# Kernel tuning notes

Hardware: AMD Instinct MI355X
Metric: run time of the kernel (lower is better)

Reference implementation:

```python
import jax, jax.numpy as jnp
import numpy as np

B, S, D, H, DK, DV = 4, 1024, 1024, 16, 64, 64
EPS = 1e-6


def _cv_layernorm(xr, xi, g_rr, g_ri, g_ii, b_r, b_i):
    # complex layernorm via 2x2 covariance whitening (Deep Complex Networks style)
    mr = xr.mean(-1, keepdims=True)
    mi = xi.mean(-1, keepdims=True)
    r = xr - mr
    i = xi - mi
    Vrr = (r * r).mean(-1, keepdims=True) + EPS
    Vii = (i * i).mean(-1, keepdims=True) + EPS
    Vri = (r * i).mean(-1, keepdims=True)
    s = jnp.sqrt(Vrr * Vii - Vri * Vri)        # sqrt(det V)
    t = jnp.sqrt(Vrr + Vii + 2.0 * s)
    inv = 1.0 / (s * t)
    Wrr = (Vii + s) * inv
    Wii = (Vrr + s) * inv
    Wri = -Vri * inv
    or_ = Wrr * r + Wri * i
    oi = Wri * r + Wii * i
    return g_rr * or_ + g_ri * oi + b_r, g_ri * or_ + g_ii * oi + b_i


def _forward(q_r, q_i, k_r, k_i, v_r, v_i, wq_r, wq_i, wk_r, wk_i, wv_r, wv_i,
             fc_r, fc_i, gamma_rr, gamma_ri, gamma_ii, beta_r, beta_i):
    qc_in = (q_r + 1j * q_i).astype(jnp.complex64)
    kc = (k_r + 1j * k_i).astype(jnp.complex64)
    vc = (v_r + 1j * v_i).astype(jnp.complex64)
    wq = (wq_r + 1j * wq_i).astype(jnp.complex64)
    wk = (wk_r + 1j * wk_i).astype(jnp.complex64)
    wv = (wv_r + 1j * wv_i).astype(jnp.complex64)
    fc = (fc_r + 1j * fc_i).astype(jnp.complex64)

    # complex QKV projections (torch Linear: y = x @ W.T), split into heads
    q = (qc_in @ wq.T).reshape(B, S, H, DK).transpose(0, 2, 1, 3)  # [B,H,S,DK]
    k = (kc @ wk.T).reshape(B, S, H, DK).transpose(0, 2, 1, 3)
    v = (vc @ wv.T).reshape(B, S, H, DV).transpose(0, 2, 1, 3)

    temp = jnp.float32(DK ** 0.5)
    attn = jnp.einsum('bhqd,bhkd->bhqk', q / temp, k)  # complex [B,H,S,S]

    # MagMinMaxNorm over last dim: min-max normalize magnitude, keep phase
    mag = jnp.abs(attn)
    mn = mag.min(-1, keepdims=True)
    mx = mag.max(-1, keepdims=True)
    scale = (mag - mn) / ((mx - mn) * mag + 1e-12)
    attn = attn * scale

    o = jnp.einsum('bhqk,bhkd->bhqd', attn, v)
    o = o.transpose(0, 2, 1, 3).reshape(B, S, H * DV)  # [B,S,H*DV]
    o = o @ fc.T
    o = o + qc_in  # residual
    out_r, out_i = _cv_layernorm(o.real, o.imag, gamma_rr, gamma_ri, gamma_ii, beta_r, beta_i)
    return jnp.stack([out_r, out_i])  # [2,B,S,D]


def setup_inputs() -> dict:
    key = jax.random.key(0)
    ks = jax.random.split(key, 14)
    rn = lambda k, shape, sc=1.0: jax.random.normal(k, shape, jnp.float32) * sc
    ws = 1.0 / np.sqrt(D)
    return {
        'q_r': rn(ks[0], (B, S, D)), 'q_i': rn(ks[1], (B, S, D)),
        'k_r': rn(ks[2], (B, S, D)), 'k_i': rn(ks[3], (B, S, D)),
        'v_r': rn(ks[4], (B, S, D)), 'v_i': rn(ks[5], (B, S, D)),
        'wq_r': rn(ks[6], (H * DK, D), ws), 'wq_i': rn(ks[7], (H * DK, D), ws),
        'wk_r': rn(ks[8], (H * DK, D), ws), 'wk_i': rn(ks[9], (H * DK, D), ws),
        'wv_r': rn(ks[10], (H * DV, D), ws), 'wv_i': rn(ks[11], (H * DV, D), ws),
        'fc_r': rn(ks[12], (D, H * DV), ws), 'fc_i': rn(ks[13], (D, H * DV), ws),
        'gamma_rr': jnp.ones((D,), jnp.float32), 'gamma_ri': jnp.zeros((D,), jnp.float32),
        'gamma_ii': jnp.ones((D,), jnp.float32),
        'beta_r': jnp.zeros((D,), jnp.float32), 'beta_i': jnp.zeros((D,), jnp.float32),
    }


def reference(q_r, q_i, k_r, k_i, v_r, v_i, wq_r, wq_i, wk_r, wk_i, wv_r, wv_i,
              fc_r, fc_i, gamma_rr, gamma_ri, gamma_ii, beta_r, beta_i):
    return _forward(q_r, q_i, k_r, k_i, v_r, v_i, wq_r, wq_i, wk_r, wk_i, wv_r, wv_i,
                    fc_r, fc_i, gamma_rr, gamma_ri, gamma_ii, beta_r, beta_i)
```

## Files before the change

### kernel.cpp

```cpp
#include <hip/hip_runtime.h>
#include <hip/hip_bf16.h>

#define BB 4
#define SS 1024
#define DD 1024
#define HH 16
#define DKH 64
#define EPS_LN 1e-6f

#define M_ROWS 4096
#define KK 2048

typedef float  floatx4 __attribute__((ext_vector_type(4)));
typedef short  shortx8 __attribute__((ext_vector_type(8)));
#define MFMA16(a, b, c) __builtin_amdgcn_mfma_f32_16x16x32_bf16(a, b, c, 0, 0, 0)

__device__ __forceinline__ unsigned pk2(float lo, float hi) {
    unsigned u;
    asm("v_cvt_pk_bf16_f32 %0, %1, %2" : "=v"(u) : "v"(lo), "v"(hi));
    return u;
}

__device__ __forceinline__ ushort f2b(float x) {
    return (ushort)(pk2(x, x) & 0xffffu);
}

__device__ __forceinline__ shortx8 negf(shortx8 x) {
    shortx8 r;
    #pragma unroll
    for (int i = 0; i < 8; ++i) r[i] = (short)(x[i] ^ (short)0x8000);
    return r;
}

__device__ __forceinline__ shortx8 vswap(shortx8 v) {
    union { shortx8 s; unsigned u[4]; } a, b;
    a.s = v;
    #pragma unroll
    for (int i = 0; i < 4; ++i) {
        const unsigned w = a.u[i];
        b.u[i] = ((w >> 16) | (w << 16)) ^ 0x00008000u;
    }
    return b.s;
}

__device__ __forceinline__ void gl16(const void* g, void* l) {
    __builtin_amdgcn_global_load_lds(
        (const __attribute__((address_space(1))) unsigned int*)g,
        (__attribute__((address_space(3))) unsigned int*)l, 16, 0, 0);
}

__global__ __launch_bounds__(256) void pack_x(
    const float* __restrict__ qr, const float* __restrict__ qi,
    const float* __restrict__ kr, const float* __restrict__ ki,
    const float* __restrict__ vr, const float* __restrict__ vi,
    ushort* __restrict__ Xq, ushort* __restrict__ Xk, ushort* __restrict__ Xv)
{
    const int t = blockIdx.y;
    const float* pr = t == 0 ? qr : t == 1 ? kr : vr;
    const float* pi = t == 0 ? qi : t == 1 ? ki : vi;
    ushort* X = t == 0 ? Xq : t == 1 ? Xk : Xv;
    const int idx = blockIdx.x * 256 + threadIdx.x;
    const int row = idx >> 8, c4 = (idx & 255) * 4;
    float4 a = *(const float4*)(pr + (size_t)row * 1024 + c4);
    float4 b = *(const float4*)(pi + (size_t)row * 1024 + c4);
    ushort4 ua; ua.x = f2b(a.x); ua.y = f2b(a.y); ua.z = f2b(a.z); ua.w = f2b(a.w);
    ushort4 ub; ub.x = f2b(b.x); ub.y = f2b(b.y); ub.z = f2b(b.z); ub.w = f2b(b.w);
    *(ushort4*)(X + (size_t)row * KK + c4)        = ua;
    *(ushort4*)(X + (size_t)row * KK + 1024 + c4) = ub;
}

__global__ __launch_bounds__(256) void pack_w(
    const float* __restrict__ ar, const float* __restrict__ ai,
    const float* __restrict__ br, const float* __restrict__ bi,
    const float* __restrict__ cr, const float* __restrict__ ci,
    const float* __restrict__ dr, const float* __restrict__ di,
    ushort* __restrict__ Bq, ushort* __restrict__ Bk,
    ushort* __restrict__ Bv, ushort* __restrict__ Bf)
{
    const int t = blockIdx.y;
    const float* wr = t == 0 ? ar : t == 1 ? br : t == 2 ? cr : dr;
    const float* wi = t == 0 ? ai : t == 1 ? bi : t == 2 ? ci : di;
    ushort* Bo = t == 0 ? Bq : t == 1 ? Bk : t == 2 ? Bv : Bf;
    const int idx = blockIdx.x * 256 + threadIdx.x;
    const int n = idx >> 8, c4 = (idx & 255) * 4;
    float4 a = *(const float4*)(wr + (size_t)n * 1024 + c4);
    float4 b = *(const float4*)(wi + (size_t)n * 1024 + c4);
    ushort4 ua; ua.x = f2b(a.x);  ua.y = f2b(a.y);  ua.z = f2b(a.z);  ua.w = f2b(a.w);
    ushort4 ub; ub.x = f2b(b.x);  ub.y = f2b(b.y);  ub.z = f2b(b.z);  ub.w = f2b(b.w);
    ushort4 un; un.x = f2b(-b.x); un.y = f2b(-b.y); un.z = f2b(-b.z); un.w = f2b(-b.w);
    *(ushort4*)(Bo + (size_t)n * KK + c4)                 = ua;
    *(ushort4*)(Bo + (size_t)n * KK + 1024 + c4)          = un;
    *(ushort4*)(Bo + (size_t)(1024 + n) * KK + c4)        = ub;
    *(ushort4*)(Bo + (size_t)(1024 + n) * KK + 1024 + c4) = ua;
}

#define GBM 128
#define GBN 256
#define GBK 64

#define GSTAGE(P, KT) do {                                                    \
    const ushort* ga_ = gA + (KT) * GBK;                                      \
    const ushort* gb_ = gB + (KT) * GBK;                                      \
    ushort* la_ = &As[P][st8];                                                \
    ushort* lb_ = &Bs[P][st8];                                                \
    gl16(ga_,                la_);                                            \
    gl16(ga_ + 64 * KK,      la_ + 4096);                                     \
    gl16(gb_,                lb_);                                            \
    gl16(gb_ + 64 * KK,      lb_ + 4096);                                     \
    gl16(gb_ + 128 * KK,     lb_ + 8192);                                     \
    gl16(gb_ + 192 * KK,     lb_ + 12288);                                    \
} while (0)

#define GKSTEP(P, VM, DOSTAGE) do {                                           \
    asm volatile("s_waitcnt vmcnt(" #VM ")" ::: "memory");                    \
    __builtin_amdgcn_s_barrier();                                             \
    __builtin_amdgcn_sched_barrier(0);                                        \
    const ushort* Ap = As[P];                                                 \
    const ushort* Bp = Bs[P];                                                 \
    shortx8 a[4][2], b[4][2];                                                 \
    _Pragma("unroll")                                                         \
    for (int f = 0; f < 4; ++f) {                                             \
        const int ra = (wm + f * 16 + l15) * GBK;                             \
        const int rb = (wn + f * 16 + l15) * GBK;                             \
        a[f][0] = *(const shortx8*)&Ap[ra + ca0];                             \
        a[f][1] = *(const shortx8*)&Ap[ra + ca1];                             \
        b[f][0] = *(const shortx8*)&Bp[rb + ca0];                             \
        b[f][1] = *(const shortx8*)&Bp[rb + ca1];                             \
    }                                                                         \
    __builtin_amdgcn_s_setprio(1);                                            \
    _Pragma("unroll")                                                         \
    for (int fm = 0; fm < 4; ++fm)                                            \
        _Pragma("unroll")                                                     \
        for (int fn = 0; fn < 4; ++fn) {                                      \
            acc[fm][fn] = MFMA16(a[fm][0], b[fn][0], acc[fm][fn]);            \
            acc[fm][fn] = MFMA16(a[fm][1], b[fn][1], acc[fm][fn]);            \
        }                                                                     \
    __builtin_amdgcn_s_setprio(0);                                            \
    asm volatile("s_waitcnt lgkmcnt(0)" ::: "memory");                        \
    __builtin_amdgcn_sched_barrier(0);                                        \
    __builtin_amdgcn_s_barrier();                                             \
    if (DOSTAGE) GSTAGE(P, kt + 2);                                           \
    ++kt;                                                                     \
} while (0)

__device__ __forceinline__ void bgemm_body(
    const ushort* __restrict__ A, const ushort* __restrict__ Bm,
    void* __restrict__ out0, void* __restrict__ out1,
    const float* __restrict__ resr, const float* __restrict__ resi,
    float scale, int mode, int bx, int by)
{
    __shared__ __align__(16) ushort As[2][GBM * GBK];
    __shared__ __align__(16) ushort Bs[2][GBN * GBK];

    const int t = threadIdx.x;
    const int lane = t & 63, wave = t >> 6;
    const int l15 = lane & 15, quad = lane >> 4;
    const int wm = (wave >> 2) * 64;
    const int wn = (wave & 3) * 64;
    const int m0 = by * GBM, n0 = bx * GBN;

    const int srow = t >> 3;
    const int schk = (t & 7) ^ (srow & 7);
    const int st8  = t * 8;
    const ushort* gA = A  + (size_t)(m0 + srow) * KK + schk * 8;
    const ushort* gB = Bm + (size_t)(n0 + srow) * KK + schk * 8;

    const int rm  = l15 & 7;
    const int ca0 = ((quad)     ^ rm) * 8;
    const int ca1 = ((4 + quad) ^ rm) * 8;

    floatx4 acc[4][4];
    #pragma unroll
    for (int fm = 0; fm < 4; ++fm)
        #pragma unroll
        for (int fn = 0; fn < 4; ++fn)
            acc[fm][fn] = (floatx4){0.f, 0.f, 0.f, 0.f};

    GSTAGE(0, 0);
    GSTAGE(1, 1);

    int kt = 0;
    for (int i = 0; i < 15; ++i) {
        GKSTEP(0, 6, 1);
        GKSTEP(1, 6, 1);
    }
    GKSTEP(0, 6, 0);
    GKSTEP(1, 0, 0);

    #pragma unroll
    for (int fm = 0; fm < 4; ++fm) {
        #pragma unroll
        for (int fn = 0; fn < 4; ++fn) {
            #pragma unroll
            for (int r = 0; r < 4; ++r) {
                const int m = m0 + wm + fm * 16 + quad * 4 + r;
                const int n = n0 + wn + fn * 16 + l15;
                const float v = acc[fm][fn][r] * scale;
                const int nn = n & 1023;
                const int hh = nn >> 6;
                const int bb = m >> 10, s = m & 1023;
                if (mode == 0) {
                    const int dk = (n < 1024 ? 0 : 64) + (nn & 63);
                    const int tq = s >> 5, row = s & 31;
                    ushort* Qb = (ushort*)out0 +
                        ((size_t)(bb * HH + hh) * 32 + tq) * 4096;
                    const int off = ((row >> 4) * 4 + (dk >> 5)) * 512 +
                                    ((dk >> 3) & 3) * 128 + (row & 15) * 8 + (dk & 7);
                    Qb[off] = f2b(v);
                } else if (mode == 3) {
                    const int dk = (n < 1024 ? 0 : 64) + (nn & 63);
                    const int tt = s >> 6, row = s & 63;
                    ushort* Kb = (ushort*)out0 +
                        ((size_t)(bb * HH + hh) * 16 + tt) * 8192;
                    const int off = ((row >> 4) * 4 + (dk >> 5)) * 512 +
                                    ((dk >> 3) & 3) * 128 + (row & 15) * 8 + (dk & 7);
                    Kb[off] = f2b(v);
                } else if (mode == 1) {
                    const int dv = nn & 63;
                    const int c = 2 * s + (n < 1024 ? 0 : 1);
                    ushort* Vb = (ushort*)out0 + (size_t)(bb * HH + hh) * 131072;
                    const int off = (((c >> 7) * 4 + (dv >> 4)) * 4 + ((c >> 5) & 3)) * 512 +
                                    ((c >> 3) & 3) * 128 + (dv & 15) * 8 + (c & 7);
                    Vb[off] = f2b(n < 1024 ? v : -v);
                } else {
                    const size_t off = (size_t)m * 1024 + nn;
                    if (n < 1024) ((float*)out0)[off] = v + resr[off];
                    else          ((float*)out1)[off] = v + resi[off];
                }
            }
        }
    }
}

__global__ __launch_bounds__(512) void bgemm_qk(
    const ushort* __restrict__ Xq, const ushort* __restrict__ Xk,
    const ushort* __restrict__ Bq, const ushort* __restrict__ Bk,
    ushort* __restrict__ qpk, ushort* __restrict__ kpk)
{
    const int z = blockIdx.z;
    bgemm_body(z == 0 ? Xq : Xk, z == 0 ? Bq : Bk,
               z == 0 ? (void*)qpk : (void*)kpk, nullptr, nullptr, nullptr,
               z == 0 ? 0.125f : 1.0f, z == 0 ? 0 : 3, blockIdx.x, blockIdx.y);
}

__global__ __launch_bounds__(512) void bgemm_v(
    const ushort* __restrict__ Xv, const ushort* __restrict__ Bv,
    ushort* __restrict__ Vneg)
{
    bgemm_body(Xv, Bv, (void*)Vneg, nullptr, nullptr, nullptr,
               1.0f, 1, blockIdx.x, blockIdx.y);
}

__global__ __launch_bounds__(512) void bgemm_fc(
    const ushort* __restrict__ A, const ushort* __restrict__ Bm,
    float* __restrict__ fr, float* __restrict__ fi,
    const float* __restrict__ resr, const float* __restrict__ resi)
{
    bgemm_body(A, Bm, fr, fi, resr, resi, 1.0f, 2, blockIdx.x, blockIdx.y);
}

#define SWZ(row, col) (((row) << 5) + ((col) ^ (((row) & 7) << 2)))

__device__ __forceinline__ void loadK(shortx8 (&K)[2][4], const ushort* kfb,
                                      int t, int kt_w) {
    #pragma unroll
    for (int kt2 = 0; kt2 < 2; ++kt2)
        #pragma unroll
        for (int f = 0; f < 4; ++f)
            K[kt2][f] = *(const shortx8*)(kfb + t * 8192 +
                                          ((kt_w * 2 + kt2) * 4 + f) * 512);
}

__device__ __forceinline__ void loadVn(shortx8 (&V)[4], const ushort* vfb,
                                       int t, int wave) {
    #pragma unroll
    for (int f = 0; f < 4; ++f)
        V[f] = *(const shortx8*)(vfb + ((t * 4 + wave) * 4 + f) * 512);
}

#define ATTN_ITER(IT, NX, KC, KN)                                             \
  {                                                                           \
    loadVn(V_, vfb, (IT), wave);                                              \
    const int p_ = (IT) & 1;                                                  \
    unsigned* Ab = Abuf[p_][kt_w];                                            \
    unsigned* Pb = Pbuf[p_][kt_w];                                            \
    floatx4 cr[2], ci[2];                                                     \
    _Pragma("unroll")                                                         \
    for (int kt2 = 0; kt2 < 2; ++kt2) {                                       \
      floatx4 r_ = (floatx4){0.f, 0.f, 0.f, 0.f};                             \
      floatx4 i_ = (floatx4){0.f, 0.f, 0.f, 0.f};                             \
      r_ = MFMA16(Aq0, KC[kt2][0], r_); r_ = MFMA16(Aq1, KC[kt2][1], r_);     \
      r_ = MFMA16(Nq2, KC[kt2][2], r_); r_ = MFMA16(Nq3, KC[kt2][3], r_);     \
      i_ = MFMA16(Aq2, KC[kt2][0], i_); i_ = MFMA16(Aq3, KC[kt2][1], i_);     \
      i_ = MFMA16(Aq0, KC[kt2][2], i_); i_ = MFMA16(Aq1, KC[kt2][3], i_);     \
      cr[kt2] = r_; ci[kt2] = i_;                                             \
    }                                                                         \
    loadK(KN, kfb, (NX), kt_w);                                               \
    _Pragma("unroll")                                                         \
    for (int kt2 = 0; kt2 < 2; ++kt2) {                                       \
      _Pragma("unroll")                                                       \
      for (int r = 0; r < 4; ++r) {                                           \
        const float ar = cr[kt2][r], ai = ci[kt2][r];                         \
        const float s2 = fmaf(ar, ar, ai * ai);                               \
        const float irm = s2 > 0.f ? rsqrtf(s2) : 0.f;                        \
        const float mag = s2 * irm;                                           \
        rmn[r] = fminf(rmn[r], mag);                                          \
        rmx[r] = fmaxf(rmx[r], mag);                                          \
        const int row_ = qt_w * 16 + quad * 4 + r;                            \
        const int w_ = SWZ(row_, kt2 * 16 + l15);                             \
        Ab[w_] = pk2(ar, ai);                                                 \
        Pb[w_] = pk2(ar * irm, ai * irm);                                     \
      }                                                                       \
    }                                                                         \
    asm volatile("s_waitcnt lgkmcnt(0)" ::: "memory");                        \
    __builtin_amdgcn_s_barrier();                                             \
    const shortx8 Vs0 = vswap(V_[0]), Vs1 = vswap(V_[1]);                     \
    const shortx8 Vs2 = vswap(V_[2]), Vs3 = vswap(V_[3]);                     \
    const unsigned* A0 = Abuf[p_][0];                                         \
    const unsigned* A1 = Abuf[p_][1];                                         \
    const unsigned* P0 = Pbuf[p_][0];                                         \
    const unsigned* P1 = Pbuf[p_][1];                                         \
    __builtin_amdgcn_s_setprio(1);                                            \
    _Pragma("unroll")                                                         \
    for (int q2 = 0; q2 < 2; ++q2) {                                          \
      const int row_ = q2 * 16 + l15;                                         \
      const int rb_ = row_ * 32, rm_ = (row_ & 7) << 2;                       \
      const int c0_ = rb_ + ((quad * 4) ^ rm_);                               \
      const int c1_ = rb_ + ((16 + quad * 4) ^ rm_);                          \
      shortx8 Af0 = *(const shortx8*)&A0[c0_];                                \
      shortx8 Af1 = *(const shortx8*)&A0[c1_];                                \
      shortx8 Af2 = *(const shortx8*)&A1[c0_];                                \
      shortx8 Af3 = *(const shortx8*)&A1[c1_];                                \
      shortx8 Pf0 = *(const shortx8*)&P0[c0_];                                \
      shortx8 Pf1 = *(const shortx8*)&P0[c1_];                                \
      shortx8 Pf2 = *(const shortx8*)&P1[c0_];                                \
      shortx8 Pf3 = *(const shortx8*)&P1[c1_];                                \
      acc[q2][0] = MFMA16(Af0, V_[0], acc[q2][0]);                            \
      acc[q2][0] = MFMA16(Af1, V_[1], acc[q2][0]);                            \
      acc[q2][0] = MFMA16(Af2, V_[2], acc[q2][0]);                            \
      acc[q2][0] = MFMA16(Af3, V_[3], acc[q2][0]);                            \
      acc[q2][1] = MFMA16(Af0, Vs0, acc[q2][1]);                              \
      acc[q2][1] = MFMA16(Af1, Vs1, acc[q2][1]);                              \
      acc[q2][1] = MFMA16(Af2, Vs2, acc[q2][1]);                              \
      acc[q2][1] = MFMA16(Af3, Vs3, acc[q2][1]);                              \
      acc[q2][2] = MFMA16(Pf0, V_[0], acc[q2][2]);                            \
      acc[q2][2] = MFMA16(Pf1, V_[1], acc[q2][2]);                            \
      acc[q2][2] = MFMA16(Pf2, V_[2], acc[q2][2]);                            \
      acc[q2][2] = MFMA16(Pf3, V_[3], acc[q2][2]);                            \
      acc[q2][3] = MFMA16(Pf0, Vs0, acc[q2][3]);                              \
      acc[q2][3] = MFMA16(Pf1, Vs1, acc[q2][3]);                              \
      acc[q2][3] = MFMA16(Pf2, Vs2, acc[q2][3]);                              \
      acc[q2][3] = MFMA16(Pf3, Vs3, acc[q2][3]);                              \
    }                                                                         \
    __builtin_amdgcn_s_setprio(0);                                            \
  }

__global__ __launch_bounds__(256) void attn_mfma(
    const ushort* __restrict__ qpk, const ushort* __restrict__ kpk,
    const ushort* __restrict__ vn, ushort* __restrict__ xo)
{
    __shared__ unsigned Abuf[2][2][32 * 32];
    __shared__ unsigned Pbuf[2][2][32 * 32];
    __shared__ unsigned mnb[32], mxb[32];

    const int tid  = threadIdx.x;
    const int wave = tid >> 6, lane = tid & 63;
    const int l15  = lane & 15, quad = lane >> 4;
    const int qt_w = wave & 1, kt_w = wave >> 1;

    const int swz = (blockIdx.x & 7) * 256 + (blockIdx.x >> 3);
    const int qt = swz & 31, hb = swz >> 5;
    const int h = hb & 15, b = hb >> 4;
    const size_t qrow0 = (size_t)b * SS + (size_t)qt * 32;

    if (tid < 32) { mnb[tid] = 0x7f800000u; mxb[tid] = 0u; }

    const ushort* qfb = qpk + ((size_t)(b * HH + h) * 32 + qt) * 4096 + lane * 8;
    shortx8 Aq0 = *(const shortx8*)(qfb + (qt_w * 4 + 0) * 512);
    shortx8 Aq1 = *(const shortx8*)(qfb + (qt_w * 4 + 1) * 512);
    shortx8 Aq2 = *(const shortx8*)(qfb + (qt_w * 4 + 2) * 512);
    shortx8 Aq3 = *(const shortx8*)(qfb + (qt_w * 4 + 3) * 512);
    shortx8 Nq2 = negf(Aq2), Nq3 = negf(Aq3);

    const ushort* kfb = kpk + (size_t)(b * HH + h) * 131072 + lane * 8;
    const ushort* vfb = vn  + (size_t)(b * HH + h) * 131072 + lane * 8;

    floatx4 acc[2][4];
    #pragma unroll
    for (int q2 = 0; q2 < 2; ++q2)
        #pragma unroll
        for (int j = 0; j < 4; ++j)
            acc[q2][j] = (floatx4){0.f, 0.f, 0.f, 0.f};
    float rmn[4] = {1e30f, 1e30f, 1e30f, 1e30f};
    float rmx[4] = {0.f, 0.f, 0.f, 0.f};

    shortx8 KA[2][4], KB[2][4], V_[4];
    loadK(KA, kfb, 0, kt_w);

    for (int it = 0; it < 16; it += 2) {
        ATTN_ITER(it,     it + 1,        KA, KB);
        ATTN_ITER(it + 1, (it + 2) & 15, KB, KA);
    }

    #pragma unroll
    for (int r = 0; r < 4; ++r) {
        float mn = rmn[r], mx = rmx[r];
        #pragma unroll
        for (int o = 1; o < 16; o <<= 1) {
            mn = fminf(mn, __shfl_xor(mn, o));
            mx = fmaxf(mx, __shfl_xor(mx, o));
        }
        if (l15 == 0) {
            const int q = qt_w * 16 + quad * 4 + r;
            atomicMin(&mnb[q], __float_as_uint(mn));
            atomicMax(&mxb[q], __float_as_uint(mx));
        }
    }
    __syncthreads();

    #pragma unroll
    for (int q2 = 0; q2 < 2; ++q2) {
        #pragma unroll
        for (int r = 0; r < 4; ++r) {
            const int q = q2 * 16 + quad * 4 + r;
            const float mn = __uint_as_float(mnb[q]);
            const float mx = __uint_as_float(mxb[q]);
            const float d = mx - mn;
            const float invd = d > 0.f ? 1.f / d : 0.f;
            const float vr_ = (acc[q2][0][r] - mn * acc[q2][2][r]) * invd;
            const float vi_ = (acc[q2][1][r] - mn * acc[q2][3][r]) * invd;
            const size_t row = (qrow0 + q) * KK + h * 64 + wave * 16 + l15;
            xo[row]        = f2b(vr_);
            xo[row + 1024] = f2b(vi_);
        }
    }
}

__global__ __launch_bounds__(256) void ln_kernel(
    const float* __restrict__ xr, const float* __restrict__ xi,
    const float* __restrict__ g_rr, const float* __restrict__ g_ri,
    const float* __restrict__ g_ii,
    const float* __restrict__ b_r, const float* __restrict__ b_i,
    float* __restrict__ out)
{
    const int lane = threadIdx.x & 63;
    const int wave = threadIdx.x >> 6;
    const int row  = blockIdx.x * 4 + wave;
    const float* pr = xr + (size_t)row * DD;
    const float* pi = xi + (size_t)row * DD;

    float r[16], im[16];
    float sr = 0.f, si = 0.f;
    #pragma unroll
    for (int j = 0; j < 16; ++j) {
        r[j]  = pr[lane + 64*j];
        im[j] = pi[lane + 64*j];
        sr += r[j]; si += im[j];
    }
    #pragma unroll
    for (int o = 32; o; o >>= 1) { sr += __shfl_xor(sr, o); si += __shfl_xor(si, o); }
    const float mr = sr * (1.f / DD), mi = si * (1.f / DD);

    float srr = 0.f, sii = 0.f, sri = 0.f;
    #pragma unroll
    for (int j = 0; j < 16; ++j) {
        const float a = r[j] - mr, c = im[j] - mi;
        srr = fmaf(a, a, srr); sii = fmaf(c, c, sii); sri = fmaf(a, c, sri);
    }
    #pragma unroll
    for (int o = 32; o; o >>= 1) {
        srr += __shfl_xor(srr, o); sii += __shfl_xor(sii, o); sri += __shfl_xor(sri, o);
    }
    const float Vrr = srr * (1.f / DD) + EPS_LN;
    const float Vii = sii * (1.f / DD) + EPS_LN;
    const float Vri = sri * (1.f / DD);
    const float s  = sqrtf(Vrr * Vii - Vri * Vri);
    const float t  = sqrtf(Vrr + Vii + 2.f * s);
    const float inv = 1.f / (s * t);
    const float Wrr = (Vii + s) * inv;
    const float Wii = (Vrr + s) * inv;
    const float Wri = -Vri * inv;

    #pragma unroll
    for (int j = 0; j < 16; ++j) {
        const int d = lane + 64*j;
        const float a = r[j] - mr, c = im[j] - mi;
        const float or_ = Wrr * a + Wri * c;
        const float oi_ = Wri * a + Wii * c;
        out[(size_t)row * DD + d] = g_rr[d]*or_ + g_ri[d]*oi_ + b_r[d];
        out[(size_t)(M_ROWS) * DD + (size_t)row * DD + d] = g_ri[d]*or_ + g_ii[d]*oi_ + b_i[d];
    }
}

extern "C" void kernel_launch(void* const* d_in, const int* in_sizes, int n_in,
                              void* d_out, int out_size, void* d_ws, size_t ws_size,
                              hipStream_t stream) {
    const float* q_r  = (const float*)d_in[0];
    const float* q_i  = (const float*)d_in[1];
    const float* k_r  = (const float*)d_in[2];
    const float* k_i  = (const float*)d_in[3];
    const float* v_r  = (const float*)d_in[4];
    const float* v_i  = (const float*)d_in[5];
    const float* wq_r = (const float*)d_in[6];
    const float* wq_i = (const float*)d_in[7];
    const float* wk_r = (const float*)d_in[8];
    const float* wk_i = (const float*)d_in[9];
    const float* wv_r = (const float*)d_in[10];
    const float* wv_i = (const float*)d_in[11];
    const float* fc_r = (const float*)d_in[12];
    const float* fc_i = (const float*)d_in[13];
    const float* g_rr = (const float*)d_in[14];
    const float* g_ri = (const float*)d_in[15];
    const float* g_ii = (const float*)d_in[16];
    const float* b_r  = (const float*)d_in[17];
    const float* b_i  = (const float*)d_in[18];
    float* out = (float*)d_out;

    float* ws = (float*)d_ws;
    const size_t NE = (size_t)M_ROWS * 1024;
    ushort* Xq   = (ushort*)(ws + 0 * NE);
    ushort* Xk   = (ushort*)(ws + 1 * NE);
    ushort* Xv   = (ushort*)(ws + 2 * NE);
    ushort* qpk  = (ushort*)(ws + 3 * NE);
    ushort* kpk  = (ushort*)(ws + 4 * NE);
    ushort* Bq   = (ushort*)(ws + 5 * NE);
    ushort* Bk   = Bq + (size_t)KK * KK;
    ushort* Bv   = (ushort*)(ws + 6 * NE);
    ushort* Bf   = Bv + (size_t)KK * KK;
    ushort* Vneg = (ushort*)(ws + 0 * NE);
    ushort* xo   = (ushort*)(ws + 2 * NE);
    float*  fr   = ws + 3 * NE;
    float*  fi   = ws + 4 * NE;

    pack_x<<<dim3(4096, 3), 256, 0, stream>>>(q_r, q_i, k_r, k_i, v_r, v_i, Xq, Xk, Xv);
    pack_w<<<dim3(1024, 4), 256, 0, stream>>>(wq_r, wq_i, wk_r, wk_i, wv_r, wv_i,
                                              fc_r, fc_i, Bq, Bk, Bv, Bf);

    bgemm_qk<<<dim3(KK / GBN, M_ROWS / GBM, 2), 512, 0, stream>>>(
        Xq, Xk, Bq, Bk, qpk, kpk);

    bgemm_v<<<dim3(KK / GBN, M_ROWS / GBM), 512, 0, stream>>>(Xv, Bv, Vneg);

    attn_mfma<<<dim3(2048), 256, 0, stream>>>(qpk, kpk, Vneg, xo);

    bgemm_fc<<<dim3(KK / GBN, M_ROWS / GBM), 512, 0, stream>>>(xo, Bf, fr, fi, q_r, q_i);

    ln_kernel<<<M_ROWS / 4, 256, 0, stream>>>(fr, fi, g_rr, g_ri, g_ii, b_r, b_i, out);
}
```

Baseline: 509.0 us.

## Enlarge GEMM tile to 256x256 with phased LDS reads and fuse QKV launch

```diff
diff --git a/kernel.cpp b/kernel.cpp
--- a/kernel.cpp
+++ b/kernel.cpp
@@ -94,52 +94,100 @@
     *(ushort4*)(Bo + (size_t)(1024 + n) * KK + 1024 + c4) = ua;
 }
 
-#define GBM 128
+#define GBM 256
 #define GBN 256
 #define GBK 64
 
-#define GSTAGE(P, KT) do {                                                    \
-    const ushort* ga_ = gA + (KT) * GBK;                                      \
-    const ushort* gb_ = gB + (KT) * GBK;                                      \
+#define STAGE8(P, T) do {                                                     \
+    const ushort* ga_ = gA + (size_t)(T) * GBK;                               \
+    const ushort* gb_ = gB + (size_t)(T) * GBK;                               \
     ushort* la_ = &As[P][st8];                                                \
     ushort* lb_ = &Bs[P][st8];                                                \
-    gl16(ga_,                la_);                                            \
-    gl16(ga_ + 64 * KK,      la_ + 4096);                                     \
-    gl16(gb_,                lb_);                                            \
-    gl16(gb_ + 64 * KK,      lb_ + 4096);                                     \
-    gl16(gb_ + 128 * KK,     lb_ + 8192);                                     \
-    gl16(gb_ + 192 * KK,     lb_ + 12288);                                    \
+    _Pragma("unroll")                                                         \
+    for (int s_ = 0; s_ < 4; ++s_)                                            \
+        gl16(ga_ + (size_t)s_ * 64 * KK, la_ + s_ * 4096);                    \
+    _Pragma("unroll")                                                         \
+    for (int s_ = 0; s_ < 4; ++s_)                                            \
+        gl16(gb_ + (size_t)s_ * 64 * KK, lb_ + s_ * 4096);                    \
 } while (0)
 
-#define GKSTEP(P, VM, DOSTAGE) do {                                           \
+#define TILE8(P, VM, DOSTAGE) do {                                            \
     asm volatile("s_waitcnt vmcnt(" #VM ")" ::: "memory");                    \
     __builtin_amdgcn_s_barrier();                                             \
+                                                                 \
+    _Pragma("unroll")                                                         \
+    for (int j = 0; j < 4; ++j) {                                             \
+        const int ra_ = aoff + j * 1024;                                      \
+        aA[j][0] = *(const shortx8*)&As[P][ra_ + ca0];                        \
+        aA[j][1] = *(const shortx8*)&As[P][ra_ + ca1];                        \
+    }                                                                         \
+    _Pragma("unroll")                                                         \
+    for (int j = 0; j < 2; ++j) {                                             \
+        const int rb_ = boff + j * 1024;                                      \
+        bA[j][0] = *(const shortx8*)&Bs[P][rb_ + ca0];                        \
+        bA[j][1] = *(const shortx8*)&Bs[P][rb_ + ca1];                        \
+    }                                                                         \
+    asm volatile("s_waitcnt lgkmcnt(0)" ::: "memory");                        \
     __builtin_amdgcn_sched_barrier(0);                                        \
-    const ushort* Ap = As[P];                                                 \
-    const ushort* Bp = Bs[P];                                                 \
-    shortx8 a[4][2], b[4][2];                                                 \
-    _Pragma("unroll")                                                         \
-    for (int f = 0; f < 4; ++f) {                                             \
-        const int ra = (wm + f * 16 + l15) * GBK;                             \
-        const int rb = (wn + f * 16 + l15) * GBK;                             \
-        a[f][0] = *(const shortx8*)&Ap[ra + ca0];                             \
-        a[f][1] = *(const shortx8*)&Ap[ra + ca1];                             \
-        b[f][0] = *(const shortx8*)&Bp[rb + ca0];                             \
-        b[f][1] = *(const shortx8*)&Bp[rb + ca1];                             \
-    }                                                                         \
     __builtin_amdgcn_s_setprio(1);                                            \
     _Pragma("unroll")                                                         \
-    for (int fm = 0; fm < 4; ++fm)                                            \
+    for (int j = 0; j < 4; ++j)                                               \
         _Pragma("unroll")                                                     \
-        for (int fn = 0; fn < 4; ++fn) {                                      \
-            acc[fm][fn] = MFMA16(a[fm][0], b[fn][0], acc[fm][fn]);            \
-            acc[fm][fn] = MFMA16(a[fm][1], b[fn][1], acc[fm][fn]);            \
+        for (int n_ = 0; n_ < 2; ++n_) {                                      \
+            acc[j][n_] = MFMA16(aA[j][0], bA[n_][0], acc[j][n_]);             \
+            acc[j][n_] = MFMA16(aA[j][1], bA[n_][1], acc[j][n_]);             \
         }                                                                     \
     __builtin_amdgcn_s_setprio(0);                                            \
+    __builtin_amdgcn_s_barrier();                                             \
+                                                                 \
+    _Pragma("unroll")                                                         \
+    for (int j = 0; j < 2; ++j) {                                             \
+        const int rb_ = boff + 2048 + j * 1024;                               \
+        bB[j][0] = *(const shortx8*)&Bs[P][rb_ + ca0];                        \
+        bB[j][1] = *(const shortx8*)&Bs[P][rb_ + ca1];                        \
+    }                                                                         \
     asm volatile("s_waitcnt lgkmcnt(0)" ::: "memory");                        \
     __builtin_amdgcn_sched_barrier(0);                                        \
+    __builtin_amdgcn_s_setprio(1);                                            \
+    _Pragma("unroll")                                                         \
+    for (int j = 0; j < 4; ++j)                                               \
+        _Pragma("unroll")                                                     \
+        for (int n_ = 0; n_ < 2; ++n_) {                                      \
+            acc[j][2 + n_] = MFMA16(aA[j][0], bB[n_][0], acc[j][2 + n_]);     \
+            acc[j][2 + n_] = MFMA16(aA[j][1], bB[n_][1], acc[j][2 + n_]);     \
+        }                                                                     \
+    __builtin_amdgcn_s_setprio(0);                                            \
     __builtin_amdgcn_s_barrier();                                             \
-    if (DOSTAGE) GSTAGE(P, kt + 2);                                           \
+                                                                 \
+    _Pragma("unroll")                                                         \
+    for (int j = 0; j < 4; ++j) {                                             \
+        const int ra_ = aoff + 4096 + j * 1024;                               \
+        aA[j][0] = *(const shortx8*)&As[P][ra_ + ca0];                        \
+        aA[j][1] = *(const shortx8*)&As[P][ra_ + ca1];                        \
+    }                                                                         \
+    asm volatile("s_waitcnt lgkmcnt(0)" ::: "memory");                        \
+    __builtin_amdgcn_sched_barrier(0);                                        \
+    __builtin_amdgcn_s_setprio(1);                                            \
+    _Pragma("unroll")                                                         \
+    for (int j = 0; j < 4; ++j)                                               \
+        _Pragma("unroll")                                                     \
+        for (int n_ = 0; n_ < 2; ++n_) {                                      \
+            acc[4 + j][2 + n_] = MFMA16(aA[j][0], bB[n_][0], acc[4 + j][2 + n_]); \
+            acc[4 + j][2 + n_] = MFMA16(aA[j][1], bB[n_][1], acc[4 + j][2 + n_]); \
+        }                                                                     \
+    __builtin_amdgcn_s_setprio(0);                                            \
+    __builtin_amdgcn_s_barrier();                                             \
+                     \
+    if (DOSTAGE) STAGE8(P, kt + 2);                                           \
+    __builtin_amdgcn_s_setprio(1);                                            \
+    _Pragma("unroll")                                                         \
+    for (int j = 0; j < 4; ++j)                                               \
+        _Pragma("unroll")                                                     \
+        for (int n_ = 0; n_ < 2; ++n_) {                                      \
+            acc[4 + j][n_] = MFMA16(aA[j][0], bA[n_][0], acc[4 + j][n_]);     \
+            acc[4 + j][n_] = MFMA16(aA[j][1], bA[n_][1], acc[4 + j][n_]);     \
+        }                                                                     \
+    __builtin_amdgcn_s_setprio(0);                                            \
     ++kt;                                                                     \
 } while (0)
 
@@ -155,7 +203,7 @@
     const int t = threadIdx.x;
     const int lane = t & 63, wave = t >> 6;
     const int l15 = lane & 15, quad = lane >> 4;
-    const int wm = (wave >> 2) * 64;
+    const int wm = (wave >> 2) * 128;
     const int wn = (wave & 3) * 64;
     const int m0 = by * GBM, n0 = bx * GBN;
 
@@ -168,27 +216,31 @@
     const int rm  = l15 & 7;
     const int ca0 = ((quad)     ^ rm) * 8;
     const int ca1 = ((4 + quad) ^ rm) * 8;
-
-    floatx4 acc[4][4];
-    #pragma unroll
-    for (int fm = 0; fm < 4; ++fm)
+    const int aoff = (wm + l15) * 64;
+    const int boff = (wn + l15) * 64;
+
+    floatx4 acc[8][4];
+    #pragma unroll
+    for (int fm = 0; fm < 8; ++fm)
         #pragma unroll
         for (int fn = 0; fn < 4; ++fn)
             acc[fm][fn] = (floatx4){0.f, 0.f, 0.f, 0.f};
 
-    GSTAGE(0, 0);
-    GSTAGE(1, 1);
+    shortx8 aA[4][2], bA[2][2], bB[2][2];
+
+    STAGE8(0, 0);
+    STAGE8(1, 1);
 
     int kt = 0;
     for (int i = 0; i < 15; ++i) {
-        GKSTEP(0, 6, 1);
-        GKSTEP(1, 6, 1);
-    }
-    GKSTEP(0, 6, 0);
-    GKSTEP(1, 0, 0);
-
-    #pragma unroll
-    for (int fm = 0; fm < 4; ++fm) {
+        TILE8(0, 8, 1);
+        TILE8(1, 8, 1);
+    }
+    TILE8(0, 8, 0);
+    TILE8(1, 0, 0);
+
+    #pragma unroll
+    for (int fm = 0; fm < 8; ++fm) {
         #pragma unroll
         for (int fn = 0; fn < 4; ++fn) {
             #pragma unroll
@@ -232,23 +284,22 @@
     }
 }
 
-__global__ __launch_bounds__(512) void bgemm_qk(
+__global__ __launch_bounds__(512) void bgemm_qkv(
     const ushort* __restrict__ Xq, const ushort* __restrict__ Xk,
+    const ushort* __restrict__ Xv,
     const ushort* __restrict__ Bq, const ushort* __restrict__ Bk,
-    ushort* __restrict__ qpk, ushort* __restrict__ kpk)
+    const ushort* __restrict__ Bv,
+    ushort* __restrict__ qpk, ushort* __restrict__ kpk,
+    ushort* __restrict__ Vneg)
 {
     const int z = blockIdx.z;
-    bgemm_body(z == 0 ? Xq : Xk, z == 0 ? Bq : Bk,
-               z == 0 ? (void*)qpk : (void*)kpk, nullptr, nullptr, nullptr,
-               z == 0 ? 0.125f : 1.0f, z == 0 ? 0 : 3, blockIdx.x, blockIdx.y);
-}
-
-__global__ __launch_bounds__(512) void bgemm_v(
-    const ushort* __restrict__ Xv, const ushort* __restrict__ Bv,
-    ushort* __restrict__ Vneg)
-{
-    bgemm_body(Xv, Bv, (void*)Vneg, nullptr, nullptr, nullptr,
-               1.0f, 1, blockIdx.x, blockIdx.y);
+    const ushort* A  = z == 0 ? Xq : z == 1 ? Xk : Xv;
+    const ushort* Bm = z == 0 ? Bq : z == 1 ? Bk : Bv;
+    void* o0 = z == 0 ? (void*)qpk : z == 1 ? (void*)kpk : (void*)Vneg;
+    const float sc = z == 0 ? 0.125f : 1.0f;
+    const int mode = z == 0 ? 0 : z == 1 ? 3 : 1;
+    bgemm_body(A, Bm, o0, nullptr, nullptr, nullptr, sc, mode,
+               blockIdx.x, blockIdx.y);
 }
 
 __global__ __launch_bounds__(512) void bgemm_fc(
@@ -527,7 +578,7 @@
     ushort* Bk   = Bq + (size_t)KK * KK;
     ushort* Bv   = (ushort*)(ws + 6 * NE);
     ushort* Bf   = Bv + (size_t)KK * KK;
-    ushort* Vneg = (ushort*)(ws + 0 * NE);
+    ushort* Vneg = (ushort*)d_out;
     ushort* xo   = (ushort*)(ws + 2 * NE);
     float*  fr   = ws + 3 * NE;
     float*  fi   = ws + 4 * NE;
@@ -536,10 +587,8 @@
     pack_w<<<dim3(1024, 4), 256, 0, stream>>>(wq_r, wq_i, wk_r, wk_i, wv_r, wv_i,
                                               fc_r, fc_i, Bq, Bk, Bv, Bf);
 
-    bgemm_qk<<<dim3(KK / GBN, M_ROWS / GBM, 2), 512, 0, stream>>>(
-        Xq, Xk, Bq, Bk, qpk, kpk);
-
-    bgemm_v<<<dim3(KK / GBN, M_ROWS / GBM), 512, 0, stream>>>(Xv, Bv, Vneg);
+    bgemm_qkv<<<dim3(KK / GBN, M_ROWS / GBM, 3), 512, 0, stream>>>(
+        Xq, Xk, Xv, Bq, Bk, Bv, qpk, kpk, Vneg);
 
     attn_mfma<<<dim3(2048), 256, 0, stream>>>(qpk, kpk, Vneg, xo);
 
```

After: 530.1 us. +4.1%, slower.

## Deepen GEMM pipeline to 4 stages with register double-buffering and merge QKV launches

Applied to the files above, without the earlier changes.

```diff
diff --git a/kernel.cpp b/kernel.cpp
--- a/kernel.cpp
+++ b/kernel.cpp
@@ -94,53 +94,51 @@
     *(ushort4*)(Bo + (size_t)(1024 + n) * KK + 1024 + c4) = ua;
 }
 
-#define GBM 128
-#define GBN 256
-#define GBK 64
-
-#define GSTAGE(P, KT) do {                                                    \
-    const ushort* ga_ = gA + (KT) * GBK;                                      \
-    const ushort* gb_ = gB + (KT) * GBK;                                      \
-    ushort* la_ = &As[P][st8];                                                \
-    ushort* lb_ = &Bs[P][st8];                                                \
-    gl16(ga_,                la_);                                            \
-    gl16(ga_ + 64 * KK,      la_ + 4096);                                     \
-    gl16(gb_,                lb_);                                            \
-    gl16(gb_ + 64 * KK,      lb_ + 4096);                                     \
-    gl16(gb_ + 128 * KK,     lb_ + 8192);                                     \
-    gl16(gb_ + 192 * KK,     lb_ + 12288);                                    \
+#define GBM 256
+#define GBN 128
+#define GBK 32
+#define ASLOT (GBM * GBK)
+#define BSLOT (GBN * GBK)
+
+#define GSTG(S) do {                                                          \
+    const int sl_ = (S) & 3;                                                  \
+    const ushort* ga_ = gA0 + (S) * GBK;                                      \
+    const ushort* gb_ = gB0 + (S) * GBK;                                      \
+    ushort* la_ = AsAll + sl_ * ASLOT + t8;                                   \
+    ushort* lb_ = BsAll + sl_ * BSLOT + t8;                                   \
+    gl16(ga_, la_);                                                           \
+    gl16(ga_ + 128 * KK, la_ + 4096);                                         \
+    gl16(gb_, lb_);                                                           \
 } while (0)
 
-#define GKSTEP(P, VM, DOSTAGE) do {                                           \
+#define GRD(J, AN, BN) do {                                                   \
+    const ushort* As_ = AsAll + ((J) & 3) * ASLOT + ard;                      \
+    const ushort* Bs_ = BsAll + ((J) & 3) * BSLOT + brd;                      \
+    AN[0] = *(const shortx8*)(As_);                                           \
+    AN[1] = *(const shortx8*)(As_ + 16 * GBK);                                \
+    AN[2] = *(const shortx8*)(As_ + 32 * GBK);                                \
+    AN[3] = *(const shortx8*)(As_ + 48 * GBK);                                \
+    BN[0] = *(const shortx8*)(Bs_);                                           \
+    BN[1] = *(const shortx8*)(Bs_ + 16 * GBK);                                \
+    BN[2] = *(const shortx8*)(Bs_ + 32 * GBK);                                \
+    BN[3] = *(const shortx8*)(Bs_ + 48 * GBK);                                \
+} while (0)
+
+#define GBODY(J, VM, DOSTAGE, DOREAD, AC, BC, AN, BN) do {                    \
+    if (DOREAD) GRD((J) + 1, AN, BN);                                         \
+    if (DOSTAGE) GSTG((J) + 4);                                               \
+    __builtin_amdgcn_sched_barrier(0);                                        \
+    __builtin_amdgcn_s_setprio(1);                                            \
+    _Pragma("unroll")                                                         \
+    for (int f_ = 0; f_ < 4; ++f_)                                            \
+        _Pragma("unroll")                                                     \
+        for (int g_ = 0; g_ < 4; ++g_)                                        \
+            acc[f_][g_] = MFMA16(AC[f_], BC[g_], acc[f_][g_]);                \
+    __builtin_amdgcn_s_setprio(0);                                            \
+    __builtin_amdgcn_sched_barrier(0);                                        \
+    asm volatile("s_waitcnt lgkmcnt(0)" ::: "memory");                        \
     asm volatile("s_waitcnt vmcnt(" #VM ")" ::: "memory");                    \
     __builtin_amdgcn_s_barrier();                                             \
-    __builtin_amdgcn_sched_barrier(0);                                        \
-    const ushort* Ap = As[P];                                                 \
-    const ushort* Bp = Bs[P];                                                 \
-    shortx8 a[4][2], b[4][2];                                                 \
-    _Pragma("unroll")                                                         \
-    for (int f = 0; f < 4; ++f) {                                             \
-        const int ra = (wm + f * 16 + l15) * GBK;                             \
-        const int rb = (wn + f * 16 + l15) * GBK;                             \
-        a[f][0] = *(const shortx8*)&Ap[ra + ca0];                             \
-        a[f][1] = *(const shortx8*)&Ap[ra + ca1];                             \
-        b[f][0] = *(const shortx8*)&Bp[rb + ca0];                             \
-        b[f][1] = *(const shortx8*)&Bp[rb + ca1];                             \
-    }                                                                         \
-    __builtin_amdgcn_s_setprio(1);                                            \
-    _Pragma("unroll")                                                         \
-    for (int fm = 0; fm < 4; ++fm)                                            \
-        _Pragma("unroll")                                                     \
-        for (int fn = 0; fn < 4; ++fn) {                                      \
-            acc[fm][fn] = MFMA16(a[fm][0], b[fn][0], acc[fm][fn]);            \
-            acc[fm][fn] = MFMA16(a[fm][1], b[fn][1], acc[fm][fn]);            \
-        }                                                                     \
-    __builtin_amdgcn_s_setprio(0);                                            \
-    asm volatile("s_waitcnt lgkmcnt(0)" ::: "memory");                        \
-    __builtin_amdgcn_sched_barrier(0);                                        \
-    __builtin_amdgcn_s_barrier();                                             \
-    if (DOSTAGE) GSTAGE(P, kt + 2);                                           \
-    ++kt;                                                                     \
 } while (0)
 
 __device__ __forceinline__ void bgemm_body(
@@ -149,43 +147,47 @@
     const float* __restrict__ resr, const float* __restrict__ resi,
     float scale, int mode, int bx, int by)
 {
-    __shared__ __align__(16) ushort As[2][GBM * GBK];
-    __shared__ __align__(16) ushort Bs[2][GBN * GBK];
+    __shared__ __align__(16) ushort AsAll[4 * ASLOT];
+    __shared__ __align__(16) ushort BsAll[4 * BSLOT];
 
     const int t = threadIdx.x;
     const int lane = t & 63, wave = t >> 6;
     const int l15 = lane & 15, quad = lane >> 4;
-    const int wm = (wave >> 2) * 64;
-    const int wn = (wave & 3) * 64;
+    const int wm = (wave >> 1) * 64;
+    const int wn = (wave & 1) * 64;
     const int m0 = by * GBM, n0 = bx * GBN;
 
-    const int srow = t >> 3;
-    const int schk = (t & 7) ^ (srow & 7);
-    const int st8  = t * 8;
-    const ushort* gA = A  + (size_t)(m0 + srow) * KK + schk * 8;
-    const ushort* gB = Bm + (size_t)(n0 + srow) * KK + schk * 8;
-
-    const int rm  = l15 & 7;
-    const int ca0 = ((quad)     ^ rm) * 8;
-    const int ca1 = ((4 + quad) ^ rm) * 8;
+    const int t8 = t * 8;
+    const ushort* gA0 = A  + (size_t)(m0 + (t >> 2)) * KK + (t & 3) * 8;
+    const ushort* gB0 = Bm + (size_t)(n0 + (t >> 2)) * KK + (t & 3) * 8;
+
+    const int ard = (wm + l15) * GBK + quad * 8;
+    const int brd = (wn + l15) * GBK + quad * 8;
 
     floatx4 acc[4][4];
     #pragma unroll
-    for (int fm = 0; fm < 4; ++fm)
+    for (int f = 0; f < 4; ++f)
         #pragma unroll
-        for (int fn = 0; fn < 4; ++fn)
-            acc[fm][fn] = (floatx4){0.f, 0.f, 0.f, 0.f};
-
-    GSTAGE(0, 0);
-    GSTAGE(1, 1);
-
-    int kt = 0;
-    for (int i = 0; i < 15; ++i) {
-        GKSTEP(0, 6, 1);
-        GKSTEP(1, 6, 1);
-    }
-    GKSTEP(0, 6, 0);
-    GKSTEP(1, 0, 0);
+        for (int g = 0; g < 4; ++g)
+            acc[f][g] = (floatx4){0.f, 0.f, 0.f, 0.f};
+
+    shortx8 aE[4], bE[4], aO[4], bO[4];
+
+    GSTG(0); GSTG(1); GSTG(2); GSTG(3);
+    asm volatile("s_waitcnt vmcnt(6)" ::: "memory");
+    __builtin_amdgcn_s_barrier();
+    GRD(0, aE, bE);
+    asm volatile("s_waitcnt lgkmcnt(0)" ::: "memory");
+    __builtin_amdgcn_s_barrier();
+
+    for (int j = 0; j < 60; j += 2) {
+        GBODY(j,     6, 1, 1, aE, bE, aO, bO);
+        GBODY(j + 1, 6, 1, 1, aO, bO, aE, bE);
+    }
+    GBODY(60, 3, 0, 1, aE, bE, aO, bO);
+    GBODY(61, 0, 0, 1, aO, bO, aE, bE);
+    GBODY(62, 0, 0, 1, aE, bE, aO, bO);
+    GBODY(63, 0, 0, 0, aO, bO, aE, bE);
 
     #pragma unroll
     for (int fm = 0; fm < 4; ++fm) {
@@ -232,26 +234,25 @@
     }
 }
 
-__global__ __launch_bounds__(512) void bgemm_qk(
+__global__ __launch_bounds__(512, 2) void bgemm_qkv(
     const ushort* __restrict__ Xq, const ushort* __restrict__ Xk,
+    const ushort* __restrict__ Xv,
     const ushort* __restrict__ Bq, const ushort* __restrict__ Bk,
-    ushort* __restrict__ qpk, ushort* __restrict__ kpk)
+    const ushort* __restrict__ Bv,
+    ushort* __restrict__ qpk, ushort* __restrict__ kpk,
+    ushort* __restrict__ Vneg)
 {
     const int z = blockIdx.z;
-    bgemm_body(z == 0 ? Xq : Xk, z == 0 ? Bq : Bk,
-               z == 0 ? (void*)qpk : (void*)kpk, nullptr, nullptr, nullptr,
-               z == 0 ? 0.125f : 1.0f, z == 0 ? 0 : 3, blockIdx.x, blockIdx.y);
-}
-
-__global__ __launch_bounds__(512) void bgemm_v(
-    const ushort* __restrict__ Xv, const ushort* __restrict__ Bv,
-    ushort* __restrict__ Vneg)
-{
-    bgemm_body(Xv, Bv, (void*)Vneg, nullptr, nullptr, nullptr,
-               1.0f, 1, blockIdx.x, blockIdx.y);
-}
-
-__global__ __launch_bounds__(512) void bgemm_fc(
+    const ushort* A  = z == 0 ? Xq : z == 1 ? Xk : Xv;
+    const ushort* Bm = z == 0 ? Bq : z == 1 ? Bk : Bv;
+    void* o0 = z == 0 ? (void*)qpk : z == 1 ? (void*)kpk : (void*)Vneg;
+    const float sc = z == 0 ? 0.125f : 1.0f;
+    const int mode = z == 0 ? 0 : z == 1 ? 3 : 1;
+    bgemm_body(A, Bm, o0, nullptr, nullptr, nullptr, sc, mode,
+               blockIdx.x, blockIdx.y);
+}
+
+__global__ __launch_bounds__(512, 2) void bgemm_fc(
     const ushort* __restrict__ A, const ushort* __restrict__ Bm,
     float* __restrict__ fr, float* __restrict__ fi,
     const float* __restrict__ resr, const float* __restrict__ resi)
@@ -527,7 +528,7 @@
     ushort* Bk   = Bq + (size_t)KK * KK;
     ushort* Bv   = (ushort*)(ws + 6 * NE);
     ushort* Bf   = Bv + (size_t)KK * KK;
-    ushort* Vneg = (ushort*)(ws + 0 * NE);
+    ushort* Vneg = (ushort*)d_out;
     ushort* xo   = (ushort*)(ws + 2 * NE);
     float*  fr   = ws + 3 * NE;
     float*  fi   = ws + 4 * NE;
@@ -536,10 +537,8 @@
     pack_w<<<dim3(1024, 4), 256, 0, stream>>>(wq_r, wq_i, wk_r, wk_i, wv_r, wv_i,
                                               fc_r, fc_i, Bq, Bk, Bv, Bf);
 
-    bgemm_qk<<<dim3(KK / GBN, M_ROWS / GBM, 2), 512, 0, stream>>>(
-        Xq, Xk, Bq, Bk, qpk, kpk);
-
-    bgemm_v<<<dim3(KK / GBN, M_ROWS / GBM), 512, 0, stream>>>(Xv, Bv, Vneg);
+    bgemm_qkv<<<dim3(KK / GBN, M_ROWS / GBM, 3), 512, 0, stream>>>(
+        Xq, Xk, Xv, Bq, Bk, Bv, qpk, kpk, Vneg);
 
     attn_mfma<<<dim3(2048), 256, 0, stream>>>(qpk, kpk, Vneg, xo);
 
```

Result: faster. 492.7 us (-3.2%).
